# Performance work log

Hardware: AMD Instinct MI355X
Metric: run time of the kernel (lower is better)

## Reference

```python
import jax, jax.numpy as jnp
import numpy as np

H = 768; NH = 12; NKV = 4; HD = 64; NL = 12; FULL = (2, 5, 8, 11)
V = 50304; IM = 3072; K = 4; EPS = 1e-6; THETA = 10000.0


def rmsnorm(x, w):
    return w * (x * jax.lax.rsqrt(jnp.mean(x * x, -1, keepdims=True) + EPS))


def rotate_half(x):
    return jnp.concatenate([-x[..., HD // 2:], x[..., :HD // 2]], -1)


def setup_inputs() -> dict:
    key = jax.random.key(0)
    ks = iter(jax.random.split(key, 48))
    def p(shape, s=0.02):
        return jax.random.normal(next(ks), shape, jnp.float32) * s
    NA = len(FULL); NC = NL - NA
    return dict(
        tokens=jax.random.randint(next(ks), (2, 1024), 0, V),
        embed=p((V, H)),
        qw=p((NA, H, H)), kw=p((NA, NKV * HD, H)), vw=p((NA, NKV * HD, H)), ow=p((NA, H, H)),
        qln=jnp.ones((NA, HD)), kln=jnp.ones((NA, HD)),
        a_gate=p((NA, IM, H)), a_up=p((NA, IM, H)), a_down=p((NA, H, IM)),
        a_ln1=jnp.ones((NA, H)), a_ln2=jnp.ones((NA, H)),
        conv_w=p((NC, H, K)), conv_b=jnp.zeros((NC, H)),
        in_w=p((NC, 3 * H, H)), in_b=jnp.zeros((NC, 3 * H)),
        out_w=p((NC, H, H)), out_b=jnp.zeros((NC, H)),
        c_gate=p((NC, IM, H)), c_up=p((NC, IM, H)), c_down=p((NC, H, IM)),
        c_ln1=jnp.ones((NC, H)), c_ln2=jnp.ones((NC, H)),
        final_ln=jnp.ones((H,)),
        lm_head=p((V, H)),
    )


def mlp(h, gate, up, down):
    return (jax.nn.silu(h @ gate.T) * (h @ up.T)) @ down.T


def attn_block(x, cos, sin, qw, kw, vw, ow, qln, kln, gate, up, down, ln1, ln2):
    r = x
    h = rmsnorm(x, ln1)
    B, S, _ = h.shape
    q = rmsnorm((h @ qw.T).reshape(B, S, NH, HD), qln).transpose(0, 2, 1, 3)   # [B,NH,S,HD]
    k = rmsnorm((h @ kw.T).reshape(B, S, NKV, HD), kln).transpose(0, 2, 1, 3)  # [B,NKV,S,HD]
    v = (h @ vw.T).reshape(B, S, NKV, HD).transpose(0, 2, 1, 3)
    q = q * cos + rotate_half(q) * sin
    k = k * cos + rotate_half(k) * sin
    rep = NH // NKV
    k = jnp.repeat(k, rep, axis=1)
    v = jnp.repeat(v, rep, axis=1)
    scores = jnp.einsum('bhqd,bhkd->bhqk', q, k) / jnp.sqrt(jnp.float32(HD))
    mask = jnp.triu(jnp.full((S, S), -jnp.inf, jnp.float32), 1)
    w = jax.nn.softmax(scores + mask, axis=-1)
    o = jnp.einsum('bhqk,bhkd->bhqd', w, v).transpose(0, 2, 1, 3).reshape(B, S, H)
    x = r + o @ ow.T
    r = x
    h = rmsnorm(x, ln2)
    return r + mlp(h, gate, up, down)


def conv_block(x, cw, cb, iw, ib, ow, ob, gate, up, down, ln1, ln2):
    r = x
    h = rmsnorm(x, ln1)
    BCx = (h @ iw.T + ib).transpose(0, 2, 1)   # [B, 3H, S]
    Bg, Cg, xg = jnp.split(BCx, 3, axis=1)
    Bx = Bg * xg
    # causal depthwise conv: left-pad K-1, equals torch padding=K-1 then [:S]
    conv = jax.lax.conv_general_dilated(
        Bx, cw[:, None, :], (1,), ((K - 1, 0),),
        dimension_numbers=('NCH', 'OIH', 'NCH'), feature_group_count=H) + cb[:, None]
    y = (Cg * conv).transpose(0, 2, 1)
    x = r + y @ ow.T + ob
    r = x
    h = rmsnorm(x, ln2)
    return r + mlp(h, gate, up, down)


def reference(tokens, embed, qw, kw, vw, ow, qln, kln, a_gate, a_up, a_down, a_ln1, a_ln2,
              conv_w, conv_b, in_w, in_b, out_w, out_b, c_gate, c_up, c_down, c_ln1, c_ln2,
              final_ln, lm_head):
    x = embed[tokens]
    S = tokens.shape[1]
    inv = 1.0 / (THETA ** (jnp.arange(0, HD, 2, dtype=jnp.float32) / HD))
    fr = jnp.outer(jnp.arange(S, dtype=jnp.float32), inv)
    emb = jnp.concatenate([fr, fr], -1)
    cos = jnp.cos(emb)[None, None]; sin = jnp.sin(emb)[None, None]
    ai = ci = 0
    for l in range(NL):
        if l in FULL:
            x = attn_block(x, cos, sin, qw[ai], kw[ai], vw[ai], ow[ai], qln[ai], kln[ai],
                           a_gate[ai], a_up[ai], a_down[ai], a_ln1[ai], a_ln2[ai])
            ai += 1
        else:
            x = conv_block(x, conv_w[ci], conv_b[ci], in_w[ci], in_b[ci], out_w[ci], out_b[ci],
                           c_gate[ci], c_up[ci], c_down[ci], c_ln1[ci], c_ln2[ci])
            ci += 1
    x = rmsnorm(x, final_ln)
    return x @ lm_head.T
```

## Files before the change

kernel.cpp:

```cpp
#include <hip/hip_runtime.h>
#include <math.h>

#define H_    768
#define NH_   12
#define NKV_  4
#define HD_   64
#define IM_   3072
#define IMH_  1536
#define KCONV 4
#define EPS_  1e-6f
#define B_    2
#define S_    1024
#define BS_   2048
#define V_    50304

typedef unsigned short u16;
typedef __bf16 bf16x8 __attribute__((ext_vector_type(8)));
typedef float  f32x4  __attribute__((ext_vector_type(4)));

__device__ __forceinline__ u16 f2bf(float f) {
    unsigned u = __float_as_uint(f);
    u += 0x7fffu + ((u >> 16) & 1u);
    return (u16)(u >> 16);
}
__device__ __forceinline__ float bf2f(u16 h) {
    return __uint_as_float((unsigned)h << 16);
}
__device__ __forceinline__ void sp_store(u16* __restrict__ hi, u16* __restrict__ lo,
                                         size_t i, float f) {
    u16 h = f2bf(f);
    hi[i] = h;
    lo[i] = f2bf(f - bf2f(h));
}
__device__ __forceinline__ void load_lds16(const void* g, void* l) {
    __builtin_amdgcn_global_load_lds(
        (const __attribute__((address_space(1))) void*)g,
        (__attribute__((address_space(3))) void*)l, 16, 0, 0);
}

__global__ void embed_kernel(const int* __restrict__ tok,
                             const float* __restrict__ emb,
                             float* __restrict__ x) {
    int bs = blockIdx.x;
    int t = threadIdx.x;
    int tk = tok[bs];
    const float* e = emb + (size_t)tk * H_;
    float* xr = x + (size_t)bs * H_;
    xr[t]       = e[t];
    xr[t + 256] = e[t + 256];
    xr[t + 512] = e[t + 512];
}

__global__ void rmsnorm768_split(const float* __restrict__ x,
                                 const float* __restrict__ wt,
                                 u16* __restrict__ yh, u16* __restrict__ yl) {
    int row = blockIdx.x;
    int t = threadIdx.x;
    const float* xr = x + (size_t)row * H_;
    float v0 = xr[t], v1 = xr[t + 256], v2 = xr[t + 512];
    __shared__ float red[256];
    red[t] = v0 * v0 + v1 * v1 + v2 * v2;
    __syncthreads();
    for (int o = 128; o > 0; o >>= 1) {
        if (t < o) red[t] += red[t + o];
        __syncthreads();
    }
    float inv = rsqrtf(red[0] / (float)H_ + EPS_);
    size_t base = (size_t)row * H_;
    sp_store(yh, yl, base + t,       v0 * inv * wt[t]);
    sp_store(yh, yl, base + t + 256, v1 * inv * wt[t + 256]);
    sp_store(yh, yl, base + t + 512, v2 * inv * wt[t + 512]);
}

__global__ void rmsnorm_head(float* __restrict__ x,
                             const float* __restrict__ w, int rows) {
    int lane = threadIdx.x & 63;
    int wv = threadIdx.x >> 6;
    int row = blockIdx.x * 4 + wv;
    if (row >= rows) return;
    float* xr = x + (size_t)row * HD_;
    float v = xr[lane];
    float ss = v * v;
    for (int o = 32; o > 0; o >>= 1) ss += __shfl_xor(ss, o);
    float inv = rsqrtf(ss / (float)HD_ + EPS_);
    xr[lane] = v * inv * w[lane];
}

__global__ void rope_kernel(float* __restrict__ x, int nh) {
    size_t idx = (size_t)blockIdx.x * 256 + threadIdx.x;
    size_t total = (size_t)BS_ * nh * 32;
    if (idx >= total) return;
    int d = (int)(idx & 31);
    size_t rest = idx >> 5;
    int h = (int)(rest % nh);
    size_t bs = rest / nh;
    int s = (int)(bs & (S_ - 1));
    float inv = powf(10000.0f, -(float)(2 * d) / (float)HD_);
    float ang = (float)s * inv;
    float c = cosf(ang), sn = sinf(ang);
    float* p = x + (bs * nh + h) * HD_;
    float x0 = p[d], x1 = p[d + 32];
    p[d]      = x0 * c - x1 * sn;
    p[d + 32] = x1 * c + x0 * sn;
}

__global__ __launch_bounds__(256) void attn_kernel(
        const float* __restrict__ q, const float* __restrict__ k,
        const float* __restrict__ v, u16* __restrict__ oh, u16* __restrict__ ol) {
    int row = blockIdx.x;
    int i = row & (S_ - 1);
    int h = (row >> 10) % NH_;
    int b = row / (S_ * NH_);
    int kh = h / (NH_ / NKV_);
    int t = threadIdx.x;

    __shared__ float qs[HD_];
    __shared__ float sc[S_];
    __shared__ float red[256];

    const float* qrow = q + ((size_t)(b * S_ + i) * NH_ + h) * HD_;
    if (t < HD_) qs[t] = qrow[t];
    __syncthreads();

    for (int j = t; j <= i; j += 256) {
        const float4* k4 = (const float4*)(k + ((size_t)(b * S_ + j) * NKV_ + kh) * HD_);
        float s = 0.f;
#pragma unroll
        for (int d4 = 0; d4 < HD_ / 4; d4++) {
            float4 kv = k4[d4];
            s += qs[4 * d4 + 0] * kv.x + qs[4 * d4 + 1] * kv.y +
                 qs[4 * d4 + 2] * kv.z + qs[4 * d4 + 3] * kv.w;
        }
        sc[j] = s * 0.125f;
    }
    __syncthreads();

    float m = -1e30f;
    for (int j = t; j <= i; j += 256) m = fmaxf(m, sc[j]);
    red[t] = m; __syncthreads();
    for (int off = 128; off > 0; off >>= 1) {
        if (t < off) red[t] = fmaxf(red[t], red[t + off]);
        __syncthreads();
    }
    m = red[0];
    __syncthreads();

    float ssum = 0.f;
    for (int j = t; j <= i; j += 256) {
        float e = expf(sc[j] - m);
        sc[j] = e;
        ssum += e;
    }
    red[t] = ssum; __syncthreads();
    for (int off = 128; off > 0; off >>= 1) {
        if (t < off) red[t] += red[t + off];
        __syncthreads();
    }
    float inv = 1.0f / red[0];
    __syncthreads();

    int dt = t & 63, g = t >> 6;
    float acc = 0.f;
    for (int j = g; j <= i; j += 4) {
        acc += sc[j] * v[((size_t)(b * S_ + j) * NKV_ + kh) * HD_ + dt];
    }
    red[t] = acc; __syncthreads();
    if (g == 0) {
        float r = (red[dt] + red[64 + dt] + red[128 + dt] + red[192 + dt]) * inv;
        sp_store(oh, ol, ((size_t)(b * S_ + i) * NH_ + h) * HD_ + dt, r);
    }
}

__global__ void conv_kernel(const float* __restrict__ bcx,
                            const float* __restrict__ cw,
                            const float* __restrict__ cb,
                            u16* __restrict__ yh, u16* __restrict__ yl) {
    size_t idx = (size_t)blockIdx.x * 256 + threadIdx.x;
    if (idx >= (size_t)BS_ * H_) return;
    int c = (int)(idx % H_);
    size_t bs = idx / H_;
    int s = (int)(bs & (S_ - 1));
    int b = (int)(bs >> 10);
    const float* base = bcx + (size_t)b * S_ * (3 * H_);
    float conv = cb[c];
#pragma unroll
    for (int t = 0; t < KCONV; t++) {
        int sp = s - (KCONV - 1) + t;
        if (sp >= 0) {
            float Bg = base[(size_t)sp * (3 * H_) + c];
            float xg = base[(size_t)sp * (3 * H_) + 2 * H_ + c];
            conv += cw[c * KCONV + t] * (Bg * xg);
        }
    }
    float Cg = base[(size_t)s * (3 * H_) + H_ + c];
    sp_store(yh, yl, idx, Cg * conv);
}

__global__ void wsplit(const float* __restrict__ in, u16* __restrict__ hi,
                       u16* __restrict__ lo, int cols4, int ld) {
    int c4 = blockIdx.x * 256 + threadIdx.x;
    if (c4 >= cols4) return;
    int r = blockIdx.y;
    float4 f = *(const float4*)(in + (size_t)r * ld + (size_t)c4 * 4);
    u16 h0 = f2bf(f.x), h1 = f2bf(f.y), h2 = f2bf(f.z), h3 = f2bf(f.w);
    ushort4 hv = make_ushort4(h0, h1, h2, h3);
    ushort4 lv = make_ushort4(f2bf(f.x - bf2f(h0)), f2bf(f.y - bf2f(h1)),
                              f2bf(f.z - bf2f(h2)), f2bf(f.w - bf2f(h3)));
    size_t o = ((size_t)r * cols4 + c4) * 4;
    *(ushort4*)(hi + o) = hv;
    *(ushort4*)(lo + o) = lv;
}

__global__ __launch_bounds__(256) void gemm_bf16x3(
        const u16* __restrict__ Ah, const u16* __restrict__ Al,
        const u16* __restrict__ Wh, const u16* __restrict__ Wl,
        const float* __restrict__ bias, const float* __restrict__ resid,
        float* __restrict__ C, u16* __restrict__ Sh, u16* __restrict__ Sl,
        int K, int ldc, int mode) {
    __shared__ u16 AsH[4096], AsL[4096], WsH[4096], WsL[4096];
    int tid = threadIdx.x;
    int l = tid & 63, w = tid >> 6;
    int bm = blockIdx.y << 7, bn = blockIdx.x << 7;

    int r0 = (w << 5) + (l >> 2);
    int r1 = r0 + 16;
    int c0 = ((l & 3) ^ ((r0 >> 1) & 3)) << 3;
    int c1 = ((l & 3) ^ ((r1 >> 1) & 3)) << 3;
    size_t ga0 = ((size_t)(bm + r0) * K + c0) * 2;
    size_t ga1 = ((size_t)(bm + r1) * K + c1) * 2;
    size_t gw0 = ((size_t)(bn + r0) * K + c0) * 2;
    size_t gw1 = ((size_t)(bn + r1) * K + c1) * 2;
    const char* pAh = (const char*)Ah;
    const char* pAl = (const char*)Al;
    const char* pWh = (const char*)Wh;
    const char* pWl = (const char*)Wl;
    int lo0 = w << 10;
    int lo1 = lo0 + 512;

    int lr = l & 15, g = l >> 4;
    int fc = (g ^ ((lr >> 1) & 3)) << 3;
    int wr = w >> 1, wc = w & 1;
    int sA = ((wr << 6) + lr) * 32 + fc;
    int sW = ((wc << 6) + lr) * 32 + fc;

    f32x4 acc[4][4] = {};

    for (int k0 = 0; k0 < K; k0 += 32) {
        size_t kb = (size_t)k0 << 1;
        load_lds16(pAh + ga0 + kb, &AsH[lo0]);
        load_lds16(pAh + ga1 + kb, &AsH[lo1]);
        load_lds16(pAl + ga0 + kb, &AsL[lo0]);
        load_lds16(pAl + ga1 + kb, &AsL[lo1]);
        load_lds16(pWh + gw0 + kb, &WsH[lo0]);
        load_lds16(pWh + gw1 + kb, &WsH[lo1]);
        load_lds16(pWl + gw0 + kb, &WsL[lo0]);
        load_lds16(pWl + gw1 + kb, &WsL[lo1]);
        __syncthreads();

        bf16x8 fah[4], fal[4], fwh[4], fwl[4];
#pragma unroll
        for (int m = 0; m < 4; m++) {
            fah[m] = *(const bf16x8*)&AsH[sA + m * 512];
            fal[m] = *(const bf16x8*)&AsL[sA + m * 512];
            fwh[m] = *(const bf16x8*)&WsH[sW + m * 512];
            fwl[m] = *(const bf16x8*)&WsL[sW + m * 512];
        }
#pragma unroll
        for (int m = 0; m < 4; m++)
#pragma unroll
            for (int n = 0; n < 4; n++) {
                f32x4 a = acc[m][n];
                a = __builtin_amdgcn_mfma_f32_16x16x32_bf16(fah[m], fwh[n], a, 0, 0, 0);
                a = __builtin_amdgcn_mfma_f32_16x16x32_bf16(fal[m], fwh[n], a, 0, 0, 0);
                a = __builtin_amdgcn_mfma_f32_16x16x32_bf16(fah[m], fwl[n], a, 0, 0, 0);
                acc[m][n] = a;
            }
        __syncthreads();
    }

    int gnb = bn + (wc << 6) + lr;
    int gmb = bm + (wr << 6) + (g << 2);
#pragma unroll
    for (int m = 0; m < 4; m++) {
#pragma unroll
        for (int n = 0; n < 4; n++) {
            int gn = gnb + n * 16;
            float badd = bias ? bias[gn] : 0.0f;
#pragma unroll
            for (int r = 0; r < 4; r++) {
                int gm = gmb + m * 16 + r;
                size_t idx = (size_t)gm * ldc + gn;
                float v = acc[m][n][r] + badd;
                if (mode == 0) {
                    if (resid) v += resid[idx];
                    C[idx] = v;
                } else if (mode == 1) {
                    sp_store(Sh, Sl, idx, v);
                } else {
                    float gt = bf2f(Sh[idx]) + bf2f(Sl[idx]);
                    float o = gt / (1.0f + expf(-gt)) * v;
                    sp_store(Sh, Sl, idx, o);
                }
            }
        }
    }
}

static inline void wsplit_launch(const float* wsrc, int rows, int cols, int ld,
                                 u16* hi, u16* lo, hipStream_t st) {
    int cols4 = cols / 4;
    dim3 g((cols4 + 255) / 256, rows);
    wsplit<<<g, 256, 0, st>>>(wsrc, hi, lo, cols4, ld);
}

static inline void gemm3(const u16* Ah, const u16* Al, const u16* Wh, const u16* Wl,
                         const float* bias, const float* resid, float* C,
                         u16* Sh, u16* Sl, int M, int N, int K, int ldc, int mode,
                         hipStream_t st) {
    dim3 grid(N / 128, M / 128);
    gemm_bf16x3<<<grid, 256, 0, st>>>(Ah, Al, Wh, Wl, bias, resid, C, Sh, Sl, K, ldc, mode);
}

extern "C" void kernel_launch(void* const* d_in, const int* in_sizes, int n_in,
                              void* d_out, int out_size, void* d_ws, size_t ws_size,
                              hipStream_t stream) {
    const int*   tokens  = (const int*)d_in[0];
    const float* embed   = (const float*)d_in[1];
    const float* qw      = (const float*)d_in[2];
    const float* kw      = (const float*)d_in[3];
    const float* vw      = (const float*)d_in[4];
    const float* ow      = (const float*)d_in[5];
    const float* qln     = (const float*)d_in[6];
    const float* kln     = (const float*)d_in[7];
    const float* a_gate  = (const float*)d_in[8];
    const float* a_up    = (const float*)d_in[9];
    const float* a_down  = (const float*)d_in[10];
    const float* a_ln1   = (const float*)d_in[11];
    const float* a_ln2   = (const float*)d_in[12];
    const float* conv_w  = (const float*)d_in[13];
    const float* conv_b  = (const float*)d_in[14];
    const float* in_w    = (const float*)d_in[15];
    const float* in_b    = (const float*)d_in[16];
    const float* out_w   = (const float*)d_in[17];
    const float* out_b   = (const float*)d_in[18];
    const float* c_gate  = (const float*)d_in[19];
    const float* c_up    = (const float*)d_in[20];
    const float* c_down  = (const float*)d_in[21];
    const float* c_ln1   = (const float*)d_in[22];
    const float* c_ln2   = (const float*)d_in[23];
    const float* fin_ln  = (const float*)d_in[24];
    const float* lm_head = (const float*)d_in[25];

    float* x  = (float*)d_ws;
    float* s1 = x + (size_t)BS_ * H_;
    u16* Hh = (u16*)(s1 + (size_t)BS_ * 3 * H_);
    u16* Hl = Hh + (size_t)BS_ * H_;
    u16* Gh = Hl + (size_t)BS_ * H_;
    u16* Gl = Gh + (size_t)BS_ * IMH_;
    u16* Wh = Gl + (size_t)BS_ * IMH_;
    u16* Wl = Wh + (size_t)3072 * 768;

    embed_kernel<<<BS_, 256, 0, stream>>>(tokens, embed, x);

    int ai = 0, ci = 0;
    for (int l = 0; l < 12; l++) {
        bool full = (l == 2 || l == 5 || l == 8 || l == 11);
        const float* gate_w; const float* up_w; const float* down_w;
        const float* ln2;
        if (full) {
            rmsnorm768_split<<<BS_, 256, 0, stream>>>(x, a_ln1 + (size_t)ai * H_, Hh, Hl);
            float* q = s1;
            float* k = s1 + (size_t)BS_ * H_;
            float* v = k + (size_t)BS_ * (NKV_ * HD_);
            wsplit_launch(qw + (size_t)ai * H_ * H_, H_, H_, H_, Wh, Wl, stream);
            gemm3(Hh, Hl, Wh, Wl, nullptr, nullptr, q, nullptr, nullptr,
                  BS_, H_, H_, H_, 0, stream);
            wsplit_launch(kw + (size_t)ai * NKV_ * HD_ * H_, NKV_ * HD_, H_, H_, Wh, Wl, stream);
            gemm3(Hh, Hl, Wh, Wl, nullptr, nullptr, k, nullptr, nullptr,
                  BS_, NKV_ * HD_, H_, NKV_ * HD_, 0, stream);
            wsplit_launch(vw + (size_t)ai * NKV_ * HD_ * H_, NKV_ * HD_, H_, H_, Wh, Wl, stream);
            gemm3(Hh, Hl, Wh, Wl, nullptr, nullptr, v, nullptr, nullptr,
                  BS_, NKV_ * HD_, H_, NKV_ * HD_, 0, stream);
            rmsnorm_head<<<(BS_ * NH_) / 4, 256, 0, stream>>>(q, qln + (size_t)ai * HD_, BS_ * NH_);
            rmsnorm_head<<<(BS_ * NKV_) / 4, 256, 0, stream>>>(k, kln + (size_t)ai * HD_, BS_ * NKV_);
            rope_kernel<<<(BS_ * NH_ * 32) / 256, 256, 0, stream>>>(q, NH_);
            rope_kernel<<<(BS_ * NKV_ * 32) / 256, 256, 0, stream>>>(k, NKV_);
            attn_kernel<<<B_ * NH_ * S_, 256, 0, stream>>>(q, k, v, Hh, Hl);
            wsplit_launch(ow + (size_t)ai * H_ * H_, H_, H_, H_, Wh, Wl, stream);
            gemm3(Hh, Hl, Wh, Wl, nullptr, x, x, nullptr, nullptr,
                  BS_, H_, H_, H_, 0, stream);
            gate_w = a_gate + (size_t)ai * IM_ * H_;
            up_w   = a_up   + (size_t)ai * IM_ * H_;
            down_w = a_down + (size_t)ai * H_ * IM_;
            ln2    = a_ln2  + (size_t)ai * H_;
            ai++;
        } else {
            rmsnorm768_split<<<BS_, 256, 0, stream>>>(x, c_ln1 + (size_t)ci * H_, Hh, Hl);
            wsplit_launch(in_w + (size_t)ci * 3 * H_ * H_, 3 * H_, H_, H_, Wh, Wl, stream);
            gemm3(Hh, Hl, Wh, Wl, in_b + (size_t)ci * 3 * H_, nullptr, s1, nullptr, nullptr,
                  BS_, 3 * H_, H_, 3 * H_, 0, stream);
            conv_kernel<<<(BS_ * H_) / 256, 256, 0, stream>>>(
                s1, conv_w + (size_t)ci * H_ * KCONV, conv_b + (size_t)ci * H_, Hh, Hl);
            wsplit_launch(out_w + (size_t)ci * H_ * H_, H_, H_, H_, Wh, Wl, stream);
            gemm3(Hh, Hl, Wh, Wl, out_b + (size_t)ci * H_, x, x, nullptr, nullptr,
                  BS_, H_, H_, H_, 0, stream);
            gate_w = c_gate + (size_t)ci * IM_ * H_;
            up_w   = c_up   + (size_t)ci * IM_ * H_;
            down_w = c_down + (size_t)ci * H_ * IM_;
            ln2    = c_ln2  + (size_t)ci * H_;
            ci++;
        }
        rmsnorm768_split<<<BS_, 256, 0, stream>>>(x, ln2, Hh, Hl);
        for (int hf = 0; hf < 2; hf++) {
            wsplit_launch(gate_w + (size_t)hf * IMH_ * H_, IMH_, H_, H_, Wh, Wl, stream);
            gemm3(Hh, Hl, Wh, Wl, nullptr, nullptr, nullptr, Gh, Gl,
                  BS_, IMH_, H_, IMH_, 1, stream);
            wsplit_launch(up_w + (size_t)hf * IMH_ * H_, IMH_, H_, H_, Wh, Wl, stream);
            gemm3(Hh, Hl, Wh, Wl, nullptr, nullptr, nullptr, Gh, Gl,
                  BS_, IMH_, H_, IMH_, 2, stream);
            wsplit_launch(down_w + (size_t)hf * IMH_, H_, IMH_, IM_, Wh, Wl, stream);
            gemm3(Gh, Gl, Wh, Wl, nullptr, x, x, nullptr, nullptr,
                  BS_, H_, IMH_, H_, 0, stream);
        }
    }

    rmsnorm768_split<<<BS_, 256, 0, stream>>>(x, fin_ln, Hh, Hl);
    for (int off = 0; off < V_; off += 3072) {
        int nc = (V_ - off < 3072) ? (V_ - off) : 3072;
        wsplit_launch(lm_head + (size_t)off * H_, nc, H_, H_, Wh, Wl, stream);
        gemm3(Hh, Hl, Wh, Wl, nullptr, nullptr, (float*)d_out + off, nullptr, nullptr,
              BS_, nc, H_, V_, 0, stream);
    }
}
```

Before: 10.35 ms.

## Split fp32 weights to bf16 hi/lo inside GEMM, fuse QKV, split-K down projection

Removes the separate weight-splitting kernel launches and instead loads fp32 weights into LDS and converts them to bf16 hi/lo inside the GEMM inner loop. Q, K and V are fused into one GEMM writing an interleaved 1280-wide buffer, and the attention, rmsnorm and rope kernels are adapted to strided access. MLP and lm_head run as single full-width launches, and the down projection uses split-K with atomic accumulation into the residual. This drops the extra global write and read of the weight split plus many launches. In exchange it adds per-tile conversion ALU work, doubles the LDS traffic for W, and makes the down-projection output depend on atomic ordering.

```diff
diff --git a/kernel.cpp b/kernel.cpp
--- a/kernel.cpp
+++ b/kernel.cpp
@@ -6,25 +6,26 @@
 #define NKV_  4
 #define HD_   64
 #define IM_   3072
-#define IMH_  1536
 #define KCONV 4
 #define EPS_  1e-6f
 #define B_    2
 #define S_    1024
 #define BS_   2048
 #define V_    50304
+#define QKVS  1280
 
 typedef unsigned short u16;
+typedef unsigned int   u32;
 typedef __bf16 bf16x8 __attribute__((ext_vector_type(8)));
 typedef float  f32x4  __attribute__((ext_vector_type(4)));
 
 __device__ __forceinline__ u16 f2bf(float f) {
-    unsigned u = __float_as_uint(f);
+    u32 u = __float_as_uint(f);
     u += 0x7fffu + ((u >> 16) & 1u);
     return (u16)(u >> 16);
 }
 __device__ __forceinline__ float bf2f(u16 h) {
-    return __uint_as_float((unsigned)h << 16);
+    return __uint_as_float((u32)h << 16);
 }
 __device__ __forceinline__ void sp_store(u16* __restrict__ hi, u16* __restrict__ lo,
                                          size_t i, float f) {
@@ -73,12 +74,14 @@
 }
 
 __global__ void rmsnorm_head(float* __restrict__ x,
-                             const float* __restrict__ w, int rows) {
+                             const float* __restrict__ w, int rows, int nh,
+                             int stride) {
     int lane = threadIdx.x & 63;
     int wv = threadIdx.x >> 6;
     int row = blockIdx.x * 4 + wv;
     if (row >= rows) return;
-    float* xr = x + (size_t)row * HD_;
+    int bs = row / nh, h = row % nh;
+    float* xr = x + (size_t)bs * stride + h * HD_;
     float v = xr[lane];
     float ss = v * v;
     for (int o = 32; o > 0; o >>= 1) ss += __shfl_xor(ss, o);
@@ -86,7 +89,7 @@
     xr[lane] = v * inv * w[lane];
 }
 
-__global__ void rope_kernel(float* __restrict__ x, int nh) {
+__global__ void rope_kernel(float* __restrict__ x, int nh, int stride) {
     size_t idx = (size_t)blockIdx.x * 256 + threadIdx.x;
     size_t total = (size_t)BS_ * nh * 32;
     if (idx >= total) return;
@@ -95,18 +98,17 @@
     int h = (int)(rest % nh);
     size_t bs = rest / nh;
     int s = (int)(bs & (S_ - 1));
-    float inv = powf(10000.0f, -(float)(2 * d) / (float)HD_);
+    float inv = exp2f((float)d * -0.41524101186092f);
     float ang = (float)s * inv;
     float c = cosf(ang), sn = sinf(ang);
-    float* p = x + (bs * nh + h) * HD_;
+    float* p = x + bs * stride + h * HD_;
     float x0 = p[d], x1 = p[d + 32];
     p[d]      = x0 * c - x1 * sn;
     p[d + 32] = x1 * c + x0 * sn;
 }
 
 __global__ __launch_bounds__(256) void attn_kernel(
-        const float* __restrict__ q, const float* __restrict__ k,
-        const float* __restrict__ v, u16* __restrict__ oh, u16* __restrict__ ol) {
+        const float* __restrict__ qkv, u16* __restrict__ oh, u16* __restrict__ ol) {
     int row = blockIdx.x;
     int i = row & (S_ - 1);
     int h = (row >> 10) % NH_;
@@ -118,12 +120,15 @@
     __shared__ float sc[S_];
     __shared__ float red[256];
 
-    const float* qrow = q + ((size_t)(b * S_ + i) * NH_ + h) * HD_;
+    const float* qrow = qkv + (size_t)(b * S_ + i) * QKVS + h * HD_;
     if (t < HD_) qs[t] = qrow[t];
     __syncthreads();
 
+    const float* kbase = qkv + 768 + kh * HD_;
+    const float* vbase = qkv + 1024 + kh * HD_;
+
     for (int j = t; j <= i; j += 256) {
-        const float4* k4 = (const float4*)(k + ((size_t)(b * S_ + j) * NKV_ + kh) * HD_);
+        const float4* k4 = (const float4*)(kbase + (size_t)(b * S_ + j) * QKVS);
         float s = 0.f;
 #pragma unroll
         for (int d4 = 0; d4 < HD_ / 4; d4++) {
@@ -162,7 +167,7 @@
     int dt = t & 63, g = t >> 6;
     float acc = 0.f;
     for (int j = g; j <= i; j += 4) {
-        acc += sc[j] * v[((size_t)(b * S_ + j) * NKV_ + kh) * HD_ + dt];
+        acc += sc[j] * vbase[(size_t)(b * S_ + j) * QKVS + dt];
     }
     red[t] = acc; __syncthreads();
     if (g == 0) {
@@ -196,85 +201,117 @@
     sp_store(yh, yl, idx, Cg * conv);
 }
 
-__global__ void wsplit(const float* __restrict__ in, u16* __restrict__ hi,
-                       u16* __restrict__ lo, int cols4, int ld) {
-    int c4 = blockIdx.x * 256 + threadIdx.x;
-    if (c4 >= cols4) return;
-    int r = blockIdx.y;
-    float4 f = *(const float4*)(in + (size_t)r * ld + (size_t)c4 * 4);
-    u16 h0 = f2bf(f.x), h1 = f2bf(f.y), h2 = f2bf(f.z), h3 = f2bf(f.w);
-    ushort4 hv = make_ushort4(h0, h1, h2, h3);
-    ushort4 lv = make_ushort4(f2bf(f.x - bf2f(h0)), f2bf(f.y - bf2f(h1)),
-                              f2bf(f.z - bf2f(h2)), f2bf(f.w - bf2f(h3)));
-    size_t o = ((size_t)r * cols4 + c4) * 4;
-    *(ushort4*)(hi + o) = hv;
-    *(ushort4*)(lo + o) = lv;
-}
-
 __global__ __launch_bounds__(256) void gemm_bf16x3(
         const u16* __restrict__ Ah, const u16* __restrict__ Al,
-        const u16* __restrict__ Wh, const u16* __restrict__ Wl,
+        const float* __restrict__ W, const float* __restrict__ Wk,
+        const float* __restrict__ Wv,
         const float* __restrict__ bias, const float* __restrict__ resid,
         float* __restrict__ C, u16* __restrict__ Sh, u16* __restrict__ Sl,
-        int K, int ldc, int mode) {
-    __shared__ u16 AsH[4096], AsL[4096], WsH[4096], WsL[4096];
+        int K, int kSplit, int ldc, int mode) {
+    __shared__ u16 AsH[4096], AsL[4096];
+    __shared__ float WsF[4096];
     int tid = threadIdx.x;
     int l = tid & 63, w = tid >> 6;
-    int bm = blockIdx.y << 7, bn = blockIdx.x << 7;
-
-    int r0 = (w << 5) + (l >> 2);
-    int r1 = r0 + 16;
-    int c0 = ((l & 3) ^ ((r0 >> 1) & 3)) << 3;
-    int c1 = ((l & 3) ^ ((r1 >> 1) & 3)) << 3;
-    size_t ga0 = ((size_t)(bm + r0) * K + c0) * 2;
-    size_t ga1 = ((size_t)(bm + r1) * K + c1) * 2;
-    size_t gw0 = ((size_t)(bn + r0) * K + c0) * 2;
-    size_t gw1 = ((size_t)(bn + r1) * K + c1) * 2;
+    int bx = blockIdx.x;
+    int bm = blockIdx.y << 7, bn = bx << 7;
+
+    const float* Wsel = W;
+    int bnW = bn;
+    if (Wk) {
+        if (bx >= 8)      { Wsel = Wv; bnW = bn - 1024; }
+        else if (bx >= 6) { Wsel = Wk; bnW = bn - 768; }
+    }
+
+    int kLen = K / kSplit;
+    int kBegin = blockIdx.z * kLen;
+    int kEnd = kBegin + kLen;
+
+    int ar0 = (w << 5) + (l >> 2);
+    int ar1 = ar0 + 16;
+    int ac0 = ((l & 3) ^ ((ar0 >> 1) & 3)) << 3;
+    int ac1 = ((l & 3) ^ ((ar1 >> 1) & 3)) << 3;
     const char* pAh = (const char*)Ah;
     const char* pAl = (const char*)Al;
-    const char* pWh = (const char*)Wh;
-    const char* pWl = (const char*)Wl;
-    int lo0 = w << 10;
-    int lo1 = lo0 + 512;
+    size_t ga0 = ((size_t)(bm + ar0) * K + ac0) * 2;
+    size_t ga1 = ((size_t)(bm + ar1) * K + ac1) * 2;
+    int wr0 = (w << 5) + (l >> 3);
+    int wcs = ((l & 7) ^ (l >> 3)) << 2;
+    const char* pW = (const char*)Wsel;
+    size_t gw0 = ((size_t)(bnW + wr0) * K + wcs) * 4;
+    size_t rowstep = (size_t)8 * K * 4;
+
+    int aLo = w << 10;
+    int wLo = w << 10;
 
     int lr = l & 15, g = l >> 4;
-    int fc = (g ^ ((lr >> 1) & 3)) << 3;
     int wr = w >> 1, wc = w & 1;
-    int sA = ((wr << 6) + lr) * 32 + fc;
-    int sW = ((wc << 6) + lr) * 32 + fc;
+    int sA = ((wr << 6) + lr) * 32 + ((g ^ ((lr >> 1) & 3)) << 3);
+    int sW = ((wc << 6) + lr) * 32;
+    int p0 = (((2 * g) ^ (lr & 7)) << 2);
+    int p1 = (((2 * g + 1) ^ (lr & 7)) << 2);
 
     f32x4 acc[4][4] = {};
 
-    for (int k0 = 0; k0 < K; k0 += 32) {
-        size_t kb = (size_t)k0 << 1;
-        load_lds16(pAh + ga0 + kb, &AsH[lo0]);
-        load_lds16(pAh + ga1 + kb, &AsH[lo1]);
-        load_lds16(pAl + ga0 + kb, &AsL[lo0]);
-        load_lds16(pAl + ga1 + kb, &AsL[lo1]);
-        load_lds16(pWh + gw0 + kb, &WsH[lo0]);
-        load_lds16(pWh + gw1 + kb, &WsH[lo1]);
-        load_lds16(pWl + gw0 + kb, &WsL[lo0]);
-        load_lds16(pWl + gw1 + kb, &WsL[lo1]);
+    for (int kt = kBegin; kt < kEnd; kt += 32) {
+        size_t kbA = (size_t)kt * 2, kbW = (size_t)kt * 4;
+        load_lds16(pAh + ga0 + kbA, &AsH[aLo]);
+        load_lds16(pAh + ga1 + kbA, &AsH[aLo + 512]);
+        load_lds16(pAl + ga0 + kbA, &AsL[aLo]);
+        load_lds16(pAl + ga1 + kbA, &AsL[aLo + 512]);
+        load_lds16(pW + gw0 + kbW,                &WsF[wLo]);
+        load_lds16(pW + gw0 + rowstep + kbW,      &WsF[wLo + 256]);
+        load_lds16(pW + gw0 + 2 * rowstep + kbW,  &WsF[wLo + 512]);
+        load_lds16(pW + gw0 + 3 * rowstep + kbW,  &WsF[wLo + 768]);
         __syncthreads();
 
-        bf16x8 fah[4], fal[4], fwh[4], fwl[4];
+        bf16x8 fah[4], fal[4];
 #pragma unroll
         for (int m = 0; m < 4; m++) {
             fah[m] = *(const bf16x8*)&AsH[sA + m * 512];
             fal[m] = *(const bf16x8*)&AsL[sA + m * 512];
-            fwh[m] = *(const bf16x8*)&WsH[sW + m * 512];
-            fwl[m] = *(const bf16x8*)&WsL[sW + m * 512];
-        }
-#pragma unroll
-        for (int m = 0; m < 4; m++)
-#pragma unroll
-            for (int n = 0; n < 4; n++) {
+        }
+#pragma unroll
+        for (int n = 0; n < 4; n++) {
+            f32x4 wa = *(const f32x4*)&WsF[sW + n * 512 + p0];
+            f32x4 wb = *(const f32x4*)&WsF[sW + n * 512 + p1];
+            union { u32 u[4]; bf16x8 v; } FH, FL;
+            u32 u0 = __float_as_uint(wa[0]), u1 = __float_as_uint(wa[1]);
+            u32 u2 = __float_as_uint(wa[2]), u3 = __float_as_uint(wa[3]);
+            u32 u4 = __float_as_uint(wb[0]), u5 = __float_as_uint(wb[1]);
+            u32 u6 = __float_as_uint(wb[2]), u7 = __float_as_uint(wb[3]);
+            u32 r0 = u0 + 0x7fffu + ((u0 >> 16) & 1u);
+            u32 r1 = u1 + 0x7fffu + ((u1 >> 16) & 1u);
+            u32 r2 = u2 + 0x7fffu + ((u2 >> 16) & 1u);
+            u32 r3 = u3 + 0x7fffu + ((u3 >> 16) & 1u);
+            u32 r4 = u4 + 0x7fffu + ((u4 >> 16) & 1u);
+            u32 r5 = u5 + 0x7fffu + ((u5 >> 16) & 1u);
+            u32 r6 = u6 + 0x7fffu + ((u6 >> 16) & 1u);
+            u32 r7 = u7 + 0x7fffu + ((u7 >> 16) & 1u);
+            FH.u[0] = __builtin_amdgcn_perm(r1, r0, 0x07060302u);
+            FH.u[1] = __builtin_amdgcn_perm(r3, r2, 0x07060302u);
+            FH.u[2] = __builtin_amdgcn_perm(r5, r4, 0x07060302u);
+            FH.u[3] = __builtin_amdgcn_perm(r7, r6, 0x07060302u);
+            float l0 = wa[0] - __uint_as_float(r0 & 0xffff0000u);
+            float l1 = wa[1] - __uint_as_float(r1 & 0xffff0000u);
+            float l2 = wa[2] - __uint_as_float(r2 & 0xffff0000u);
+            float l3 = wa[3] - __uint_as_float(r3 & 0xffff0000u);
+            float l4 = wb[0] - __uint_as_float(r4 & 0xffff0000u);
+            float l5 = wb[1] - __uint_as_float(r5 & 0xffff0000u);
+            float l6 = wb[2] - __uint_as_float(r6 & 0xffff0000u);
+            float l7 = wb[3] - __uint_as_float(r7 & 0xffff0000u);
+            FL.u[0] = __builtin_amdgcn_perm(__float_as_uint(l1), __float_as_uint(l0), 0x07060302u);
+            FL.u[1] = __builtin_amdgcn_perm(__float_as_uint(l3), __float_as_uint(l2), 0x07060302u);
+            FL.u[2] = __builtin_amdgcn_perm(__float_as_uint(l5), __float_as_uint(l4), 0x07060302u);
+            FL.u[3] = __builtin_amdgcn_perm(__float_as_uint(l7), __float_as_uint(l6), 0x07060302u);
+#pragma unroll
+            for (int m = 0; m < 4; m++) {
                 f32x4 a = acc[m][n];
-                a = __builtin_amdgcn_mfma_f32_16x16x32_bf16(fah[m], fwh[n], a, 0, 0, 0);
-                a = __builtin_amdgcn_mfma_f32_16x16x32_bf16(fal[m], fwh[n], a, 0, 0, 0);
-                a = __builtin_amdgcn_mfma_f32_16x16x32_bf16(fah[m], fwl[n], a, 0, 0, 0);
+                a = __builtin_amdgcn_mfma_f32_16x16x32_bf16(fah[m], FH.v, a, 0, 0, 0);
+                a = __builtin_amdgcn_mfma_f32_16x16x32_bf16(fal[m], FH.v, a, 0, 0, 0);
+                a = __builtin_amdgcn_mfma_f32_16x16x32_bf16(fah[m], FL.v, a, 0, 0, 0);
                 acc[m][n] = a;
             }
+        }
         __syncthreads();
     }
 
@@ -290,35 +327,34 @@
             for (int r = 0; r < 4; r++) {
                 int gm = gmb + m * 16 + r;
                 size_t idx = (size_t)gm * ldc + gn;
-                float v = acc[m][n][r] + badd;
+                float v = acc[m][n][r];
                 if (mode == 0) {
+                    v += badd;
                     if (resid) v += resid[idx];
                     C[idx] = v;
                 } else if (mode == 1) {
                     sp_store(Sh, Sl, idx, v);
-                } else {
+                } else if (mode == 2) {
                     float gt = bf2f(Sh[idx]) + bf2f(Sl[idx]);
                     float o = gt / (1.0f + expf(-gt)) * v;
                     sp_store(Sh, Sl, idx, o);
+                } else {
+                    if (kBegin == 0) v += badd;
+                    atomicAdd(&C[idx], v);
                 }
             }
         }
     }
 }
 
-static inline void wsplit_launch(const float* wsrc, int rows, int cols, int ld,
-                                 u16* hi, u16* lo, hipStream_t st) {
-    int cols4 = cols / 4;
-    dim3 g((cols4 + 255) / 256, rows);
-    wsplit<<<g, 256, 0, st>>>(wsrc, hi, lo, cols4, ld);
-}
-
-static inline void gemm3(const u16* Ah, const u16* Al, const u16* Wh, const u16* Wl,
+static inline void gemm3(const u16* Ah, const u16* Al, const float* W,
+                         const float* Wk, const float* Wv,
                          const float* bias, const float* resid, float* C,
-                         u16* Sh, u16* Sl, int M, int N, int K, int ldc, int mode,
-                         hipStream_t st) {
-    dim3 grid(N / 128, M / 128);
-    gemm_bf16x3<<<grid, 256, 0, st>>>(Ah, Al, Wh, Wl, bias, resid, C, Sh, Sl, K, ldc, mode);
+                         u16* Sh, u16* Sl, int M, int N, int K, int kSplit,
+                         int ldc, int mode, hipStream_t st) {
+    dim3 grid(N / 128, M / 128, kSplit);
+    gemm_bf16x3<<<grid, 256, 0, st>>>(Ah, Al, W, Wk, Wv, bias, resid, C, Sh, Sl,
+                                      K, kSplit, ldc, mode);
 }
 
 extern "C" void kernel_launch(void* const* d_in, const int* in_sizes, int n_in,
@@ -356,9 +392,7 @@
     u16* Hh = (u16*)(s1 + (size_t)BS_ * 3 * H_);
     u16* Hl = Hh + (size_t)BS_ * H_;
     u16* Gh = Hl + (size_t)BS_ * H_;
-    u16* Gl = Gh + (size_t)BS_ * IMH_;
-    u16* Wh = Gl + (size_t)BS_ * IMH_;
-    u16* Wl = Wh + (size_t)3072 * 768;
+    u16* Gl = Gh + (size_t)BS_ * IM_;
 
     embed_kernel<<<BS_, 256, 0, stream>>>(tokens, embed, x);
 
@@ -369,26 +403,20 @@
         const float* ln2;
         if (full) {
             rmsnorm768_split<<<BS_, 256, 0, stream>>>(x, a_ln1 + (size_t)ai * H_, Hh, Hl);
-            float* q = s1;
-            float* k = s1 + (size_t)BS_ * H_;
-            float* v = k + (size_t)BS_ * (NKV_ * HD_);
-            wsplit_launch(qw + (size_t)ai * H_ * H_, H_, H_, H_, Wh, Wl, stream);
-            gemm3(Hh, Hl, Wh, Wl, nullptr, nullptr, q, nullptr, nullptr,
-                  BS_, H_, H_, H_, 0, stream);
-            wsplit_launch(kw + (size_t)ai * NKV_ * HD_ * H_, NKV_ * HD_, H_, H_, Wh, Wl, stream);
-            gemm3(Hh, Hl, Wh, Wl, nullptr, nullptr, k, nullptr, nullptr,
-                  BS_, NKV_ * HD_, H_, NKV_ * HD_, 0, stream);
-            wsplit_launch(vw + (size_t)ai * NKV_ * HD_ * H_, NKV_ * HD_, H_, H_, Wh, Wl, stream);
-            gemm3(Hh, Hl, Wh, Wl, nullptr, nullptr, v, nullptr, nullptr,
-                  BS_, NKV_ * HD_, H_, NKV_ * HD_, 0, stream);
-            rmsnorm_head<<<(BS_ * NH_) / 4, 256, 0, stream>>>(q, qln + (size_t)ai * HD_, BS_ * NH_);
-            rmsnorm_head<<<(BS_ * NKV_) / 4, 256, 0, stream>>>(k, kln + (size_t)ai * HD_, BS_ * NKV_);
-            rope_kernel<<<(BS_ * NH_ * 32) / 256, 256, 0, stream>>>(q, NH_);
-            rope_kernel<<<(BS_ * NKV_ * 32) / 256, 256, 0, stream>>>(k, NKV_);
-            attn_kernel<<<B_ * NH_ * S_, 256, 0, stream>>>(q, k, v, Hh, Hl);
-            wsplit_launch(ow + (size_t)ai * H_ * H_, H_, H_, H_, Wh, Wl, stream);
-            gemm3(Hh, Hl, Wh, Wl, nullptr, x, x, nullptr, nullptr,
-                  BS_, H_, H_, H_, 0, stream);
+            gemm3(Hh, Hl, qw + (size_t)ai * H_ * H_,
+                  kw + (size_t)ai * NKV_ * HD_ * H_,
+                  vw + (size_t)ai * NKV_ * HD_ * H_,
+                  nullptr, nullptr, s1, nullptr, nullptr,
+                  BS_, QKVS, H_, 1, QKVS, 0, stream);
+            rmsnorm_head<<<(BS_ * NH_) / 4, 256, 0, stream>>>(
+                s1, qln + (size_t)ai * HD_, BS_ * NH_, NH_, QKVS);
+            rmsnorm_head<<<(BS_ * NKV_) / 4, 256, 0, stream>>>(
+                s1 + 768, kln + (size_t)ai * HD_, BS_ * NKV_, NKV_, QKVS);
+            rope_kernel<<<(BS_ * NH_ * 32) / 256, 256, 0, stream>>>(s1, NH_, QKVS);
+            rope_kernel<<<(BS_ * NKV_ * 32) / 256, 256, 0, stream>>>(s1 + 768, NKV_, QKVS);
+            attn_kernel<<<B_ * NH_ * S_, 256, 0, stream>>>(s1, Hh, Hl);
+            gemm3(Hh, Hl, ow + (size_t)ai * H_ * H_, nullptr, nullptr,
+                  nullptr, x, x, nullptr, nullptr, BS_, H_, H_, 1, H_, 0, stream);
             gate_w = a_gate + (size_t)ai * IM_ * H_;
             up_w   = a_up   + (size_t)ai * IM_ * H_;
             down_w = a_down + (size_t)ai * H_ * IM_;
@@ -396,14 +424,14 @@
             ai++;
         } else {
             rmsnorm768_split<<<BS_, 256, 0, stream>>>(x, c_ln1 + (size_t)ci * H_, Hh, Hl);
-            wsplit_launch(in_w + (size_t)ci * 3 * H_ * H_, 3 * H_, H_, H_, Wh, Wl, stream);
-            gemm3(Hh, Hl, Wh, Wl, in_b + (size_t)ci * 3 * H_, nullptr, s1, nullptr, nullptr,
-                  BS_, 3 * H_, H_, 3 * H_, 0, stream);
+            gemm3(Hh, Hl, in_w + (size_t)ci * 3 * H_ * H_, nullptr, nullptr,
+                  in_b + (size_t)ci * 3 * H_, nullptr, s1, nullptr, nullptr,
+                  BS_, 3 * H_, H_, 1, 3 * H_, 0, stream);
             conv_kernel<<<(BS_ * H_) / 256, 256, 0, stream>>>(
                 s1, conv_w + (size_t)ci * H_ * KCONV, conv_b + (size_t)ci * H_, Hh, Hl);
-            wsplit_launch(out_w + (size_t)ci * H_ * H_, H_, H_, H_, Wh, Wl, stream);
-            gemm3(Hh, Hl, Wh, Wl, out_b + (size_t)ci * H_, x, x, nullptr, nullptr,
-                  BS_, H_, H_, H_, 0, stream);
+            gemm3(Hh, Hl, out_w + (size_t)ci * H_ * H_, nullptr, nullptr,
+                  out_b + (size_t)ci * H_, x, x, nullptr, nullptr,
+                  BS_, H_, H_, 1, H_, 0, stream);
             gate_w = c_gate + (size_t)ci * IM_ * H_;
             up_w   = c_up   + (size_t)ci * IM_ * H_;
             down_w = c_down + (size_t)ci * H_ * IM_;
@@ -411,24 +439,15 @@
             ci++;
         }
         rmsnorm768_split<<<BS_, 256, 0, stream>>>(x, ln2, Hh, Hl);
-        for (int hf = 0; hf < 2; hf++) {
-            wsplit_launch(gate_w + (size_t)hf * IMH_ * H_, IMH_, H_, H_, Wh, Wl, stream);
-            gemm3(Hh, Hl, Wh, Wl, nullptr, nullptr, nullptr, Gh, Gl,
-                  BS_, IMH_, H_, IMH_, 1, stream);
-            wsplit_launch(up_w + (size_t)hf * IMH_ * H_, IMH_, H_, H_, Wh, Wl, stream);
-            gemm3(Hh, Hl, Wh, Wl, nullptr, nullptr, nullptr, Gh, Gl,
-                  BS_, IMH_, H_, IMH_, 2, stream);
-            wsplit_launch(down_w + (size_t)hf * IMH_, H_, IMH_, IM_, Wh, Wl, stream);
-            gemm3(Gh, Gl, Wh, Wl, nullptr, x, x, nullptr, nullptr,
-                  BS_, H_, IMH_, H_, 0, stream);
-        }
+        gemm3(Hh, Hl, gate_w, nullptr, nullptr, nullptr, nullptr, nullptr,
+              Gh, Gl, BS_, IM_, H_, 1, IM_, 1, stream);
+        gemm3(Hh, Hl, up_w, nullptr, nullptr, nullptr, nullptr, nullptr,
+              Gh, Gl, BS_, IM_, H_, 1, IM_, 2, stream);
+        gemm3(Gh, Gl, down_w, nullptr, nullptr, nullptr, nullptr, x,
+              nullptr, nullptr, BS_, H_, IM_, 2, H_, 3, stream);
     }
 
     rmsnorm768_split<<<BS_, 256, 0, stream>>>(x, fin_ln, Hh, Hl);
-    for (int off = 0; off < V_; off += 3072) {
-        int nc = (V_ - off < 3072) ? (V_ - off) : 3072;
-        wsplit_launch(lm_head + (size_t)off * H_, nc, H_, H_, Wh, Wl, stream);
-        gemm3(Hh, Hl, Wh, Wl, nullptr, nullptr, (float*)d_out + off, nullptr, nullptr,
-              BS_, nc, H_, V_, 0, stream);
-    }
-}
+    gemm3(Hh, Hl, lm_head, nullptr, nullptr, nullptr, nullptr, (float*)d_out,
+          nullptr, nullptr, BS_, V_, H_, 1, V_, 0, stream);
+}
```

New measurement: 8.294 ms. 19.8% less time.
